# Optimization experiments

Measured on AMD Instinct MI355X. Metric: run time of the kernel, lower is better.

The kernel has to match this reference:

```python
import jax, jax.numpy as jnp
import numpy as np
from jax import lax

CONF_THRESH = 0.5   # from module __init__
NMS_THRESH = 0.4    # from module __init__
TOP_K = 1000        # static pre-NMS candidate cap (JAX needs fixed shapes)

B, N, C = 16, 22743, 80  # batch, predictions (608px, 3 scales), COCO classes


def setup_inputs() -> dict:
    key = jax.random.key(0)
    # YOLOv3 raw output: [B, N, 5+C] = (cx, cy, w, h, obj, cls_0..cls_{C-1})
    v3_out = jax.random.uniform(key, (B, N, 5 + C), dtype=jnp.float32)
    return {"v3_out": v3_out}


def _xywh2xyxy(b):
    cx, cy, w, h = b[..., 0], b[..., 1], b[..., 2], b[..., 3]
    return jnp.stack([cx - w * 0.5, cy - h * 0.5, cx + w * 0.5, cy + h * 0.5], axis=-1)


def _pairwise_iou(boxes):
    # boxes: [K, 4] in xyxy -> [K, K] IoU
    x1 = jnp.maximum(boxes[:, None, 0], boxes[None, :, 0])
    y1 = jnp.maximum(boxes[:, None, 1], boxes[None, :, 1])
    x2 = jnp.minimum(boxes[:, None, 2], boxes[None, :, 2])
    y2 = jnp.minimum(boxes[:, None, 3], boxes[None, :, 3])
    inter = jnp.clip(x2 - x1, 0.0) * jnp.clip(y2 - y1, 0.0)
    area = jnp.clip(boxes[:, 2] - boxes[:, 0], 0.0) * jnp.clip(boxes[:, 3] - boxes[:, 1], 0.0)
    union = area[:, None] + area[None, :] - inter
    return inter / (union + 1e-16)


def _nms_image(pred):
    # pred: [N, 5+C]
    boxes = _xywh2xyxy(pred[:, :4])                 # [N, 4]
    obj = pred[:, 4]
    cls_conf = jnp.max(pred[:, 5:], axis=-1)        # best class confidence
    cls_id = jnp.argmax(pred[:, 5:], axis=-1)       # best class index
    # confidence filter (obj >= thresh) folded into the sort key
    score = jnp.where(obj >= CONF_THRESH, obj * cls_conf, -1.0)
    top_score, idx = lax.top_k(score, TOP_K)        # sorted descending by score
    valid = top_score > 0.0                          # survivors of the conf filter

    boxes_k = boxes[idx]          # [K, 4]
    obj_k = obj[idx]
    conf_k = cls_conf[idx]
    cls_k = cls_id[idx]

    iou = _pairwise_iou(boxes_k)                                   # [K, K]
    suppress = (iou > NMS_THRESH) & (cls_k[:, None] == cls_k[None, :])

    # greedy NMS over the score-sorted list: box i (if kept) kills later overlaps
    later = jnp.arange(TOP_K)

    def step(i, keep):
        kill = suppress[i] & (later > i) & keep[i]
        return keep & ~kill

    keep = lax.fori_loop(0, TOP_K, step, valid)

    # detections: (x1, y1, x2, y2, obj_conf, cls_conf, cls_id), zeroed where dropped
    dets = jnp.concatenate(
        [boxes_k, obj_k[:, None], conf_k[:, None], cls_k.astype(jnp.float32)[:, None]],
        axis=-1,
    )
    return dets * keep[:, None].astype(dets.dtype)   # [K, 7]


def reference(v3_out):
    # [B, K, 7] padded detections per image (zero rows = suppressed/invalid)
    return jax.vmap(_nms_image)(v3_out)
```

## Files before the change

### kernel.cpp

```cpp
#include <hip/hip_runtime.h>
#include <cstdint>

#pragma clang fp contract(off)

constexpr int cB = 16;
constexpr int cN = 22743;
constexpr int cROW = 85;
constexpr int cK = 1000;
constexpr float CONF_T = 0.5f;
constexpr float NMS_T = 0.4f;

__global__ __launch_bounds__(256) void k_score(const float* __restrict__ in,
                                               unsigned* __restrict__ ukey) {
  __shared__ float sdata[10880];
  constexpr int F4_PER_BLK = 2720;
  constexpr int TOTAL_F4 = (cB * cN * cROW) / 4;
  int tid = threadIdx.x;
  const float4* gin4 = (const float4*)in;
  float4* s4 = (float4*)sdata;
  int base_f4 = blockIdx.x * F4_PER_BLK;
#pragma unroll
  for (int q = 0; q < 11; ++q) {
    int k = tid + 256 * q;
    if (k < F4_PER_BLK) {
      int g = base_f4 + k;
      if (g < TOTAL_F4) s4[k] = gin4[g];
    }
  }
  __syncthreads();
  int r = tid >> 1, h = tid & 1;
  int grow = blockIdx.x * 128 + r;
  if (grow < cB * cN) {
    const float* rowp = sdata + cROW * r;
    int j0 = 5 + h * 40;
    float m0 = rowp[j0 + 0], m1 = rowp[j0 + 1];
    float m2 = rowp[j0 + 2], m3 = rowp[j0 + 3];
#pragma unroll
    for (int k = 4; k < 40; k += 4) {
      m0 = fmaxf(m0, rowp[j0 + k + 0]);
      m1 = fmaxf(m1, rowp[j0 + k + 1]);
      m2 = fmaxf(m2, rowp[j0 + k + 2]);
      m3 = fmaxf(m3, rowp[j0 + k + 3]);
    }
    float m = fmaxf(fmaxf(m0, m1), fmaxf(m2, m3));
    m = fmaxf(m, __shfl_xor(m, 1));
    if (h == 0) {
      float obj = rowp[4];
      unsigned u = 0u;
      if (obj >= CONF_T) {
        float s = obj * m;
        if (s > 0.0f) u = __float_as_uint(s);
      }
      ukey[grow] = u;
    }
  }
}

__device__ __forceinline__ void sort1024_u32_asc(unsigned* a, int tid) {
  for (int k = 2; k <= 1024; k <<= 1) {
    for (int j = k >> 1; j >= 1; j >>= 1) {
      __syncthreads();
      if (tid < 512) {
        int i = ((tid & ~(j - 1)) << 1) | (tid & (j - 1));
        int p = i | j;
        unsigned x = a[i], y = a[p];
        bool up = ((i & k) == 0);
        bool sw = up ? (x > y) : (x < y);
        if (sw) { a[i] = y; a[p] = x; }
      }
    }
  }
  __syncthreads();
}

__global__ __launch_bounds__(1024) void k_topk(const unsigned* __restrict__ ukey,
                                               int* __restrict__ topidx) {
  __shared__ unsigned hist[2048];
  __shared__ unsigned wtot[16];
  __shared__ unsigned long long cand[1024];
  __shared__ unsigned eqbuf[1024];
  __shared__ unsigned sh_T, sh_newrank, sh_E, sh_cnt;
  int img = blockIdx.x;
  int tid = threadIdx.x;
  int lane = tid & 63;
  int wv = tid >> 6;
  const unsigned* uk = ukey + (size_t)img * cN;

  constexpr int NIT = (cN + 1023) / 1024;
  unsigned uv[NIT];
#pragma unroll
  for (int q = 0; q < NIT; ++q) {
    int i = q * 1024 + tid;
    uv[q] = (i < cN) ? uk[i] : 0u;
  }

  unsigned prefix = 0;
  int bits = 0;
  unsigned rank = cK;
  unsigned gtc = 0;
  unsigned E = 0;

  for (int r = 0; r < 3; ++r) {
    int nb = (r < 2) ? 11 : 10;
    int shift = 32 - bits - nb;
    hist[tid] = 0u; hist[tid + 1024] = 0u;
    __syncthreads();
#pragma unroll
    for (int q = 0; q < NIT; ++q) {
      unsigned u = uv[q];
      bool inr = (q * 1024 + tid) < cN;
      bool match = inr && (bits == 0 || (u >> (32 - bits)) == prefix);
      bool isz = match && (u == 0u);
      bool nz = match && (u != 0u);
      unsigned long long mz = __ballot(isz);
      if (isz && lane == (__ffsll((long long)mz) - 1))
        atomicAdd(&hist[0], (unsigned)__popcll(mz));
      if (nz) atomicAdd(&hist[(u >> shift) & ((1u << nb) - 1u)], 1u);
    }
    __syncthreads();
    unsigned h0 = hist[2 * tid];
    unsigned h1 = hist[2 * tid + 1];
    unsigned s2 = h0 + h1;
#pragma unroll
    for (int s = 1; s < 64; s <<= 1) {
      unsigned t = __shfl_down(s2, s);
      s2 += (lane + s < 64) ? t : 0u;
    }
    if (lane == 0) wtot[wv] = s2;
    __syncthreads();
    unsigned above = 0;
    for (int w2 = wv + 1; w2 < 16; ++w2) above += wtot[w2];
    unsigned S_even = above + s2;
    unsigned S_odd = S_even - h0;
    unsigned S_next = S_odd - h1;
    if (S_even >= rank && S_odd < rank) { sh_T = 2u * tid; sh_newrank = rank - S_odd; sh_E = h0; }
    if (S_odd >= rank && S_next < rank) { sh_T = 2u * tid + 1u; sh_newrank = rank - S_next; sh_E = h1; }
    __syncthreads();
    unsigned T = sh_T;
    unsigned nr = sh_newrank;
    E = sh_E;
    gtc += rank - nr;
    rank = nr;
    prefix = (prefix << nb) | T;
    bits += nb;
    __syncthreads();
    if (gtc + E <= 1024u) break;
  }

  bool tiepath = (gtc + E > 1024u);
  unsigned pivotLo = (bits >= 32) ? prefix : (prefix << (32 - bits));
  cand[tid] = (unsigned long long)tid;
  eqbuf[tid] = 0xFFFFFFFFu;
  if (tid == 0) sh_cnt = 0u;
  __syncthreads();

  if (!tiepath) {
#pragma unroll
    for (int q = 0; q < NIT; ++q) {
      int i = q * 1024 + tid;
      unsigned u = uv[q];
      bool m = (i < cN) && (u >= pivotLo);
      unsigned long long mb = __ballot(m);
      if (m) {
        int ldr = __ffsll((long long)mb) - 1;
        unsigned base = 0;
        if (lane == ldr) base = atomicAdd(&sh_cnt, (unsigned)__popcll(mb));
        base = __shfl(base, ldr);
        unsigned pos = base + (unsigned)__popcll(mb & ((1ull << lane) - 1ull));
        if (pos < 1024u)
          cand[pos] = ((unsigned long long)u << 32) |
                      (unsigned long long)(0xFFFFFFFFu - (unsigned)i);
      }
    }
    __syncthreads();
  } else {
    unsigned P = prefix;
#pragma unroll
    for (int q = 0; q < NIT; ++q) {
      int i = q * 1024 + tid;
      unsigned u = uv[q];
      bool gt = (i < cN) && (u > P);
      unsigned long long mb = __ballot(gt);
      if (gt) {
        int ldr = __ffsll((long long)mb) - 1;
        unsigned base = 0;
        if (lane == ldr) base = atomicAdd(&sh_cnt, (unsigned)__popcll(mb));
        base = __shfl(base, ldr);
        unsigned pos = base + (unsigned)__popcll(mb & ((1ull << lane) - 1ull));
        if (pos < 1024u)
          cand[pos] = ((unsigned long long)u << 32) |
                      (unsigned long long)(0xFFFFFFFFu - (unsigned)i);
      }
    }
    __syncthreads();
    if (tid == 0) sh_E = 0u;
    __syncthreads();
#pragma unroll
    for (int q = 0; q < NIT; ++q) {
      int i = q * 1024 + tid;
      unsigned u = uv[q];
      bool eq = (i < cN) && (u == P);
      unsigned long long mb = __ballot(eq);
      if (eq) {
        int ldr = __ffsll((long long)mb) - 1;
        unsigned base = 0;
        if (lane == ldr) base = atomicAdd(&sh_E, (unsigned)__popcll(mb));
        base = __shfl(base, ldr);
        unsigned pos = base + (unsigned)__popcll(mb & ((1ull << lane) - 1ull));
        if (pos < 1024u) eqbuf[pos] = (unsigned)i;
      }
    }
    __syncthreads();
    sort1024_u32_asc(eqbuf, tid);
    int need = (int)cK - (int)gtc;
    for (int t = tid; t < need; t += 1024) {
      unsigned idx = eqbuf[t];
      if (idx != 0xFFFFFFFFu)
        cand[gtc + (unsigned)t] = ((unsigned long long)P << 32) |
                                  (unsigned long long)(0xFFFFFFFFu - idx);
    }
    __syncthreads();
  }

  unsigned long long my = cand[tid];
  unsigned rk = 0;
#pragma unroll 8
  for (int j = 0; j < 1024; ++j) rk += (cand[j] > my) ? 1u : 0u;
  if (rk < (unsigned)cK) {
    unsigned uhi = (unsigned)(my >> 32);
    int idx = (int)(0xFFFFFFFFu - (unsigned)(my & 0xFFFFFFFFull));
    topidx[img * cK + (int)rk] = (uhi > 0u) ? idx : -1;
  }
}

__global__ __launch_bounds__(256) void k_gather(const float* __restrict__ in,
                                                const int* __restrict__ topidx,
                                                float4* __restrict__ boxes,
                                                float* __restrict__ area,
                                                float* __restrict__ objv,
                                                float* __restrict__ confv,
                                                int* __restrict__ clsv,
                                                int* __restrict__ validv) {
  int wid = (int)((blockIdx.x * 256u + threadIdx.x) >> 6);
  int lane = threadIdx.x & 63;
  if (wid >= cB * cK) return;
  int img = wid / cK;
  int idx = topidx[wid];
  if (idx < 0) {
    if (lane == 0) {
      boxes[wid] = make_float4(0.f, 0.f, 0.f, 0.f);
      area[wid] = 0.f; objv[wid] = 0.f; confv[wid] = 0.f;
      clsv[wid] = -1; validv[wid] = 0;
    }
    return;
  }
  const float* row = in + ((size_t)img * cN + (size_t)idx) * cROW;
  float v = row[5 + lane];
  int ci = lane;
  if (lane < 16) {
    float v2 = row[69 + lane];
    if (v2 > v) { v = v2; ci = 64 + lane; }
  }
#pragma unroll
  for (int m = 1; m < 64; m <<= 1) {
    float ov = __shfl_xor(v, m);
    int oc = __shfl_xor(ci, m);
    if (ov > v || (ov == v && oc < ci)) { v = ov; ci = oc; }
  }
  if (lane == 0) {
    float cx = row[0], cy = row[1], w = row[2], h = row[3], ob = row[4];
    float hw = w * 0.5f, hh = h * 0.5f;
    float x1 = cx - hw, y1 = cy - hh, x2 = cx + hw, y2 = cy + hh;
    boxes[wid] = make_float4(x1, y1, x2, y2);
    area[wid] = fmaxf(x2 - x1, 0.f) * fmaxf(y2 - y1, 0.f);
    objv[wid] = ob; confv[wid] = v; clsv[wid] = ci; validv[wid] = 1;
  }
}

__global__ __launch_bounds__(256) void k_suppress(const float4* __restrict__ boxes,
                                                  const float* __restrict__ area,
                                                  const int* __restrict__ clsv,
                                                  unsigned* __restrict__ St) {
  __shared__ float sx1[1056], sy1[1056], sx2[1056], sy2[1056], sar[1056];
  __shared__ int scls[1056];
  int img = blockIdx.x >> 7;
  int rb = (blockIdx.x & 127) * 8;
  int tid = threadIdx.x;
  for (int i = tid; i < 1024; i += 256) {
    int p = i + (i >> 5);
    if (i < cK) {
      float4 b = boxes[img * cK + i];
      sx1[p] = b.x; sy1[p] = b.y; sx2[p] = b.z; sy2[p] = b.w;
      sar[p] = area[img * cK + i];
      scls[p] = clsv[img * cK + i];
    } else {
      sx1[p] = 0.f; sy1[p] = 0.f; sx2[p] = 0.f; sy2[p] = 0.f; sar[p] = 0.f;
      scls[p] = -2;
    }
  }
  __syncthreads();
  int i = rb + (tid >> 5);
  int w = tid & 31;
  int pi = i + (i >> 5);
  float bx1 = sx1[pi], by1 = sy1[pi], bx2 = sx2[pi], by2 = sy2[pi], ba = sar[pi];
  int bc = scls[pi];
  unsigned word = 0u;
#pragma unroll 4
  for (int bit = 0; bit < 32; ++bit) {
    int pj = 33 * w + bit;
    float xx1 = fmaxf(bx1, sx1[pj]);
    float yy1 = fmaxf(by1, sy1[pj]);
    float xx2 = fminf(bx2, sx2[pj]);
    float yy2 = fminf(by2, sy2[pj]);
    float inter = fmaxf(xx2 - xx1, 0.f) * fmaxf(yy2 - yy1, 0.f);
    float uni = ba + sar[pj] - inter;
    float iou = inter / (uni + 1e-16f);
    if (iou > NMS_T && bc == scls[pj]) word |= (1u << bit);
  }
  St[((size_t)(img * 32 + w)) * 1024 + (size_t)i] = word;
}

__device__ __forceinline__ unsigned u4c(const uint4& v, int c) {
  return c == 0 ? v.x : c == 1 ? v.y : c == 2 ? v.z : v.w;
}

__device__ __forceinline__ void nms_load(const uint4* __restrict__ colv, int b,
                                         uint4 (&buf)[8]) {
#pragma unroll
  for (int q = 0; q < 8; ++q) buf[q] = colv[8 * b + q];
}

__device__ __forceinline__ void nms_proc(int b, int lane, unsigned& kw,
                                         const uint4 (&W)[8]) {
  unsigned dec = 0u;
  if (lane == b) {
    unsigned kwb = kw;
#pragma unroll
    for (int t = 0; t < 32; ++t) {
      if ((kwb >> t) & 1u) {
        dec |= (1u << t);
        unsigned rw = u4c(W[t >> 2], t & 3);
        unsigned mgt = (t == 31) ? 0u : (0xFFFFFFFFu << (t + 1));
        kwb &= ~(rw & mgt);
      }
    }
    kw = kwb;
  }
  dec = __shfl(dec, b);
  if (lane > b) {
#pragma unroll
    for (int t = 0; t < 32; ++t) {
      unsigned sel = 0u - ((dec >> t) & 1u);
      kw &= ~(u4c(W[t >> 2], t & 3) & sel);
    }
  }
}

__global__ __launch_bounds__(64) void k_nms(const unsigned* __restrict__ St,
                                            const int* __restrict__ validv,
                                            const float4* __restrict__ boxes,
                                            const float* __restrict__ objv,
                                            const float* __restrict__ confv,
                                            const int* __restrict__ clsv,
                                            float* __restrict__ out) {
  __shared__ unsigned keep_sh[32];
  int img = blockIdx.x;
  int lane = threadIdx.x;
  if (lane < 32) {
    const uint4* colv = (const uint4*)(St + ((size_t)(img * 32 + lane)) * 1024);
    unsigned kw = 0u;
    const int4* v4 = (const int4*)(validv + img * cK);
#pragma unroll
    for (int q = 0; q < 8; ++q) {
      int k0 = (lane << 5) + 4 * q;
      if (k0 < cK) {
        int4 t = v4[lane * 8 + q];
        kw |= (unsigned)(t.x != 0) << (4 * q + 0);
        kw |= (unsigned)(t.y != 0) << (4 * q + 1);
        kw |= (unsigned)(t.z != 0) << (4 * q + 2);
        kw |= (unsigned)(t.w != 0) << (4 * q + 3);
      }
    }
    uint4 bufA[8], bufB[8];
    nms_load(colv, 0, bufA);
    for (int b = 0; b < 32; b += 2) {
      if (b + 1 < 32) nms_load(colv, b + 1, bufB);
      nms_proc(b, lane, kw, bufA);
      if (b + 2 < 32) nms_load(colv, b + 2, bufA);
      nms_proc(b + 1, lane, kw, bufB);
    }
    keep_sh[lane] = kw;
  }
  __syncthreads();
  for (int k = lane; k < cK; k += 64) {
    bool kp = ((keep_sh[k >> 5] >> (k & 31)) & 1u) != 0u;
    size_t o = ((size_t)img * cK + (size_t)k) * 7;
    if (kp) {
      float4 b = boxes[img * cK + k];
      out[o + 0] = b.x; out[o + 1] = b.y; out[o + 2] = b.z; out[o + 3] = b.w;
      out[o + 4] = objv[img * cK + k];
      out[o + 5] = confv[img * cK + k];
      out[o + 6] = (float)clsv[img * cK + k];
    } else {
      out[o + 0] = 0.f; out[o + 1] = 0.f; out[o + 2] = 0.f; out[o + 3] = 0.f;
      out[o + 4] = 0.f; out[o + 5] = 0.f; out[o + 6] = 0.f;
    }
  }
}

extern "C" void kernel_launch(void* const* d_in, const int* in_sizes, int n_in,
                              void* d_out, int out_size, void* d_ws, size_t ws_size,
                              hipStream_t stream) {
  const float* in = (const float*)d_in[0];
  float* out = (float*)d_out;
  char* ws = (char*)d_ws;
  size_t off = 0;
  auto take = [&](size_t bytes) {
    size_t r = off;
    off += (bytes + 255) & ~(size_t)255;
    return r;
  };
  unsigned* ukey = (unsigned*)(ws + take((size_t)cB * cN * 4));
  int* topidx = (int*)(ws + take((size_t)cB * cK * 4));
  float4* boxes = (float4*)(ws + take((size_t)cB * cK * 16));
  float* area = (float*)(ws + take((size_t)cB * cK * 4));
  float* objv = (float*)(ws + take((size_t)cB * cK * 4));
  float* confv = (float*)(ws + take((size_t)cB * cK * 4));
  int* clsv = (int*)(ws + take((size_t)cB * cK * 4));
  int* validv = (int*)(ws + take((size_t)cB * cK * 4));
  unsigned* St = (unsigned*)(ws + take((size_t)cB * 32 * 1024 * 4));

  int nrows = cB * cN;
  int blocks1 = (nrows + 127) / 128;
  k_score<<<blocks1, 256, 0, stream>>>(in, ukey);
  k_topk<<<cB, 1024, 0, stream>>>(ukey, topidx);
  int waves3 = cB * cK;
  k_gather<<<(waves3 * 64 + 255) / 256, 256, 0, stream>>>(in, topidx, boxes, area,
                                                          objv, confv, clsv, validv);
  k_suppress<<<cB * 128, 256, 0, stream>>>(boxes, area, clsv, St);
  k_nms<<<cB, 64, 0, stream>>>(St, validv, boxes, objv, confv, clsv, out);
}
```

Baseline: 281.0 us.

## Fuse gather into top-k and NMS into suppress via last-block atomic counter

```diff
diff --git a/kernel.cpp b/kernel.cpp
--- a/kernel.cpp
+++ b/kernel.cpp
@@ -74,17 +74,28 @@
 }
 
 __global__ __launch_bounds__(1024) void k_topk(const unsigned* __restrict__ ukey,
-                                               int* __restrict__ topidx) {
+                                               const float* __restrict__ in,
+                                               int* __restrict__ topidx,
+                                               float4* __restrict__ boxes,
+                                               float* __restrict__ area,
+                                               float* __restrict__ objv,
+                                               float* __restrict__ confv,
+                                               int* __restrict__ clsv,
+                                               unsigned* __restrict__ cnt) {
   __shared__ unsigned hist[2048];
   __shared__ unsigned wtot[16];
   __shared__ unsigned long long cand[1024];
   __shared__ unsigned eqbuf[1024];
+  __shared__ unsigned praw[8][1024];
+  __shared__ int sh_topidx[1024];
   __shared__ unsigned sh_T, sh_newrank, sh_E, sh_cnt;
   int img = blockIdx.x;
   int tid = threadIdx.x;
   int lane = tid & 63;
   int wv = tid >> 6;
   const unsigned* uk = ukey + (size_t)img * cN;
+
+  if (tid == 0) cnt[img] = 0u;
 
   constexpr int NIT = (cN + 1023) / 1024;
   unsigned uv[NIT];
@@ -222,67 +233,142 @@
     __syncthreads();
   }
 
+  {
+    int kg = wv & 7, jg = wv >> 3;
+    unsigned long long myv[8];
+#pragma unroll
+    for (int m = 0; m < 8; ++m) myv[m] = cand[jg * 512 + m * 64 + lane];
+    unsigned c[8];
+#pragma unroll
+    for (int m = 0; m < 8; ++m) c[m] = 0u;
+    int k0 = kg * 128;
+#pragma unroll 4
+    for (int k = 0; k < 128; ++k) {
+      unsigned long long ck = cand[k0 + k];
+#pragma unroll
+      for (int m = 0; m < 8; ++m) c[m] += (ck > myv[m]) ? 1u : 0u;
+    }
+#pragma unroll
+    for (int m = 0; m < 8; ++m) praw[kg][jg * 512 + m * 64 + lane] = c[m];
+  }
+  __syncthreads();
+  unsigned rk = 0;
+#pragma unroll
+  for (int g = 0; g < 8; ++g) rk += praw[g][tid];
   unsigned long long my = cand[tid];
-  unsigned rk = 0;
-#pragma unroll 8
-  for (int j = 0; j < 1024; ++j) rk += (cand[j] > my) ? 1u : 0u;
+  sh_topidx[tid] = -1;
+  __syncthreads();
   if (rk < (unsigned)cK) {
     unsigned uhi = (unsigned)(my >> 32);
     int idx = (int)(0xFFFFFFFFu - (unsigned)(my & 0xFFFFFFFFull));
-    topidx[img * cK + (int)rk] = (uhi > 0u) ? idx : -1;
-  }
-}
-
-__global__ __launch_bounds__(256) void k_gather(const float* __restrict__ in,
-                                                const int* __restrict__ topidx,
-                                                float4* __restrict__ boxes,
-                                                float* __restrict__ area,
-                                                float* __restrict__ objv,
-                                                float* __restrict__ confv,
-                                                int* __restrict__ clsv,
-                                                int* __restrict__ validv) {
-  int wid = (int)((blockIdx.x * 256u + threadIdx.x) >> 6);
-  int lane = threadIdx.x & 63;
-  if (wid >= cB * cK) return;
-  int img = wid / cK;
-  int idx = topidx[wid];
-  if (idx < 0) {
+    int oi = (uhi > 0u) ? idx : -1;
+    topidx[img * cK + (int)rk] = oi;
+    sh_topidx[(int)rk] = oi;
+  }
+  __syncthreads();
+
+  for (int j = 0; j < 32; ++j) {
+    int s0 = wv + 32 * j;
+    int s1 = s0 + 16;
+    int i0 = (s0 < cK) ? sh_topidx[s0] : -1;
+    int i1 = (s1 < cK) ? sh_topidx[s1] : -1;
+    const float* r0 = in + ((size_t)img * cN + (size_t)(i0 < 0 ? 0 : i0)) * cROW;
+    const float* r1 = in + ((size_t)img * cN + (size_t)(i1 < 0 ? 0 : i1)) * cROW;
+    float va = r0[5 + lane];
+    float vb = r1[5 + lane];
+    int ca = lane, cb = lane;
+    if (lane < 16) {
+      float v2a = r0[69 + lane];
+      float v2b = r1[69 + lane];
+      if (v2a > va) { va = v2a; ca = 64 + lane; }
+      if (v2b > vb) { vb = v2b; cb = 64 + lane; }
+    }
+#pragma unroll
+    for (int m = 1; m < 64; m <<= 1) {
+      float ova = __shfl_xor(va, m); int oca = __shfl_xor(ca, m);
+      float ovb = __shfl_xor(vb, m); int ocb = __shfl_xor(cb, m);
+      if (ova > va || (ova == va && oca < ca)) { va = ova; ca = oca; }
+      if (ovb > vb || (ovb == vb && ocb < cb)) { vb = ovb; cb = ocb; }
+    }
     if (lane == 0) {
-      boxes[wid] = make_float4(0.f, 0.f, 0.f, 0.f);
-      area[wid] = 0.f; objv[wid] = 0.f; confv[wid] = 0.f;
-      clsv[wid] = -1; validv[wid] = 0;
-    }
-    return;
-  }
-  const float* row = in + ((size_t)img * cN + (size_t)idx) * cROW;
-  float v = row[5 + lane];
-  int ci = lane;
-  if (lane < 16) {
-    float v2 = row[69 + lane];
-    if (v2 > v) { v = v2; ci = 64 + lane; }
-  }
-#pragma unroll
-  for (int m = 1; m < 64; m <<= 1) {
-    float ov = __shfl_xor(v, m);
-    int oc = __shfl_xor(ci, m);
-    if (ov > v || (ov == v && oc < ci)) { v = ov; ci = oc; }
-  }
-  if (lane == 0) {
-    float cx = row[0], cy = row[1], w = row[2], h = row[3], ob = row[4];
-    float hw = w * 0.5f, hh = h * 0.5f;
-    float x1 = cx - hw, y1 = cy - hh, x2 = cx + hw, y2 = cy + hh;
-    boxes[wid] = make_float4(x1, y1, x2, y2);
-    area[wid] = fmaxf(x2 - x1, 0.f) * fmaxf(y2 - y1, 0.f);
-    objv[wid] = ob; confv[wid] = v; clsv[wid] = ci; validv[wid] = 1;
-  }
-}
-
-__global__ __launch_bounds__(256) void k_suppress(const float4* __restrict__ boxes,
-                                                  const float* __restrict__ area,
-                                                  const int* __restrict__ clsv,
-                                                  unsigned* __restrict__ St) {
+      if (s0 < cK) {
+        int wid = img * cK + s0;
+        if (i0 < 0) {
+          boxes[wid] = make_float4(0.f, 0.f, 0.f, 0.f);
+          area[wid] = 0.f; objv[wid] = 0.f; confv[wid] = 0.f; clsv[wid] = -1;
+        } else {
+          float cx = r0[0], cy = r0[1], w = r0[2], h = r0[3], ob = r0[4];
+          float hw = w * 0.5f, hh = h * 0.5f;
+          float x1 = cx - hw, y1 = cy - hh, x2 = cx + hw, y2 = cy + hh;
+          boxes[wid] = make_float4(x1, y1, x2, y2);
+          area[wid] = fmaxf(x2 - x1, 0.f) * fmaxf(y2 - y1, 0.f);
+          objv[wid] = ob; confv[wid] = va; clsv[wid] = ca;
+        }
+      }
+      if (s1 < cK) {
+        int wid = img * cK + s1;
+        if (i1 < 0) {
+          boxes[wid] = make_float4(0.f, 0.f, 0.f, 0.f);
+          area[wid] = 0.f; objv[wid] = 0.f; confv[wid] = 0.f; clsv[wid] = -1;
+        } else {
+          float cx = r1[0], cy = r1[1], w = r1[2], h = r1[3], ob = r1[4];
+          float hw = w * 0.5f, hh = h * 0.5f;
+          float x1 = cx - hw, y1 = cy - hh, x2 = cx + hw, y2 = cy + hh;
+          boxes[wid] = make_float4(x1, y1, x2, y2);
+          area[wid] = fmaxf(x2 - x1, 0.f) * fmaxf(y2 - y1, 0.f);
+          objv[wid] = ob; confv[wid] = vb; clsv[wid] = cb;
+        }
+      }
+    }
+  }
+}
+
+__device__ __forceinline__ unsigned u4c(const uint4& v, int c) {
+  return c == 0 ? v.x : c == 1 ? v.y : c == 2 ? v.z : v.w;
+}
+
+__device__ __forceinline__ void nms_load(const uint4* __restrict__ colv, int b,
+                                         uint4 (&buf)[8]) {
+#pragma unroll
+  for (int q = 0; q < 8; ++q) buf[q] = colv[8 * b + q];
+}
+
+__device__ __forceinline__ void nms_proc(int b, int lane, unsigned& kw,
+                                         const uint4 (&W)[8]) {
+  unsigned dec = 0u;
+  if (lane == b) {
+    unsigned kwb = kw;
+#pragma unroll
+    for (int t = 0; t < 32; ++t) {
+      if ((kwb >> t) & 1u) {
+        dec |= (1u << t);
+        unsigned rw = u4c(W[t >> 2], t & 3);
+        unsigned mgt = (t == 31) ? 0u : (0xFFFFFFFFu << (t + 1));
+        kwb &= ~(rw & mgt);
+      }
+    }
+    kw = kwb;
+  }
+  dec = __shfl(dec, b);
+  if (dec != 0u && lane > b) {
+#pragma unroll
+    for (int t = 0; t < 32; ++t) {
+      unsigned sel = 0u - ((dec >> t) & 1u);
+      kw &= ~(u4c(W[t >> 2], t & 3) & sel);
+    }
+  }
+}
+
+__global__ __launch_bounds__(256) void k_suppress_nms(
+    const float4* __restrict__ boxes, const float* __restrict__ area,
+    const int* __restrict__ clsv, const float* __restrict__ objv,
+    const float* __restrict__ confv, const int* __restrict__ topidx,
+    unsigned* __restrict__ St, unsigned* __restrict__ cnt,
+    float* __restrict__ out) {
   __shared__ float sx1[1056], sy1[1056], sx2[1056], sy2[1056], sar[1056];
   __shared__ int scls[1056];
+  __shared__ unsigned sh_old;
+  __shared__ unsigned keep_sh[32];
   int img = blockIdx.x >> 7;
   int rb = (blockIdx.x & 127) * 8;
   int tid = threadIdx.x;
@@ -299,100 +385,64 @@
     }
   }
   __syncthreads();
-  int i = rb + (tid >> 5);
-  int w = tid & 31;
-  int pi = i + (i >> 5);
-  float bx1 = sx1[pi], by1 = sy1[pi], bx2 = sx2[pi], by2 = sy2[pi], ba = sar[pi];
-  int bc = scls[pi];
-  unsigned word = 0u;
+  {
+    int i = rb + (tid >> 5);
+    int w = tid & 31;
+    int pi = i + (i >> 5);
+    float bx1 = sx1[pi], by1 = sy1[pi], bx2 = sx2[pi], by2 = sy2[pi], ba = sar[pi];
+    int bc = scls[pi];
+    unsigned word = 0u;
 #pragma unroll 4
-  for (int bit = 0; bit < 32; ++bit) {
-    int pj = 33 * w + bit;
-    float xx1 = fmaxf(bx1, sx1[pj]);
-    float yy1 = fmaxf(by1, sy1[pj]);
-    float xx2 = fminf(bx2, sx2[pj]);
-    float yy2 = fminf(by2, sy2[pj]);
-    float inter = fmaxf(xx2 - xx1, 0.f) * fmaxf(yy2 - yy1, 0.f);
-    float uni = ba + sar[pj] - inter;
-    float iou = inter / (uni + 1e-16f);
-    if (iou > NMS_T && bc == scls[pj]) word |= (1u << bit);
-  }
-  St[((size_t)(img * 32 + w)) * 1024 + (size_t)i] = word;
-}
-
-__device__ __forceinline__ unsigned u4c(const uint4& v, int c) {
-  return c == 0 ? v.x : c == 1 ? v.y : c == 2 ? v.z : v.w;
-}
-
-__device__ __forceinline__ void nms_load(const uint4* __restrict__ colv, int b,
-                                         uint4 (&buf)[8]) {
-#pragma unroll
-  for (int q = 0; q < 8; ++q) buf[q] = colv[8 * b + q];
-}
-
-__device__ __forceinline__ void nms_proc(int b, int lane, unsigned& kw,
-                                         const uint4 (&W)[8]) {
-  unsigned dec = 0u;
-  if (lane == b) {
-    unsigned kwb = kw;
-#pragma unroll
-    for (int t = 0; t < 32; ++t) {
-      if ((kwb >> t) & 1u) {
-        dec |= (1u << t);
-        unsigned rw = u4c(W[t >> 2], t & 3);
-        unsigned mgt = (t == 31) ? 0u : (0xFFFFFFFFu << (t + 1));
-        kwb &= ~(rw & mgt);
-      }
-    }
-    kw = kwb;
-  }
-  dec = __shfl(dec, b);
-  if (lane > b) {
-#pragma unroll
-    for (int t = 0; t < 32; ++t) {
-      unsigned sel = 0u - ((dec >> t) & 1u);
-      kw &= ~(u4c(W[t >> 2], t & 3) & sel);
-    }
-  }
-}
-
-__global__ __launch_bounds__(64) void k_nms(const unsigned* __restrict__ St,
-                                            const int* __restrict__ validv,
-                                            const float4* __restrict__ boxes,
-                                            const float* __restrict__ objv,
-                                            const float* __restrict__ confv,
-                                            const int* __restrict__ clsv,
-                                            float* __restrict__ out) {
-  __shared__ unsigned keep_sh[32];
-  int img = blockIdx.x;
-  int lane = threadIdx.x;
-  if (lane < 32) {
-    const uint4* colv = (const uint4*)(St + ((size_t)(img * 32 + lane)) * 1024);
+    for (int bit = 0; bit < 32; ++bit) {
+      int pj = 33 * w + bit;
+      float xx1 = fmaxf(bx1, sx1[pj]);
+      float yy1 = fmaxf(by1, sy1[pj]);
+      float xx2 = fminf(bx2, sx2[pj]);
+      float yy2 = fminf(by2, sy2[pj]);
+      float inter = fmaxf(xx2 - xx1, 0.f) * fmaxf(yy2 - yy1, 0.f);
+      float uni = ba + sar[pj] - inter;
+      float iou = inter / (uni + 1e-16f);
+      if (iou > NMS_T && bc == scls[pj]) word |= (1u << bit);
+    }
+    St[((size_t)(img * 32 + w)) * 1024 + (size_t)i] = word;
+  }
+  __syncthreads();
+  if (tid == 0) {
+    __threadfence();
+    sh_old = atomicAdd(&cnt[img], 1u);
+  }
+  __syncthreads();
+  if (sh_old != 127u) return;
+  if (tid == 0) __threadfence();
+  __syncthreads();
+
+  if (tid < 32) {
+    const uint4* colv = (const uint4*)(St + ((size_t)(img * 32 + tid)) * 1024);
     unsigned kw = 0u;
-    const int4* v4 = (const int4*)(validv + img * cK);
+    const int4* v4 = (const int4*)(topidx + img * cK);
 #pragma unroll
     for (int q = 0; q < 8; ++q) {
-      int k0 = (lane << 5) + 4 * q;
+      int k0 = (tid << 5) + 4 * q;
       if (k0 < cK) {
-        int4 t = v4[lane * 8 + q];
-        kw |= (unsigned)(t.x != 0) << (4 * q + 0);
-        kw |= (unsigned)(t.y != 0) << (4 * q + 1);
-        kw |= (unsigned)(t.z != 0) << (4 * q + 2);
-        kw |= (unsigned)(t.w != 0) << (4 * q + 3);
+        int4 t = v4[tid * 8 + q];
+        kw |= (unsigned)(t.x >= 0) << (4 * q + 0);
+        kw |= (unsigned)(t.y >= 0) << (4 * q + 1);
+        kw |= (unsigned)(t.z >= 0) << (4 * q + 2);
+        kw |= (unsigned)(t.w >= 0) << (4 * q + 3);
       }
     }
     uint4 bufA[8], bufB[8];
     nms_load(colv, 0, bufA);
     for (int b = 0; b < 32; b += 2) {
       if (b + 1 < 32) nms_load(colv, b + 1, bufB);
-      nms_proc(b, lane, kw, bufA);
+      nms_proc(b, tid, kw, bufA);
       if (b + 2 < 32) nms_load(colv, b + 2, bufA);
-      nms_proc(b + 1, lane, kw, bufB);
-    }
-    keep_sh[lane] = kw;
-  }
-  __syncthreads();
-  for (int k = lane; k < cK; k += 64) {
+      nms_proc(b + 1, tid, kw, bufB);
+    }
+    keep_sh[tid] = kw;
+  }
+  __syncthreads();
+  for (int k = tid; k < cK; k += 256) {
     bool kp = ((keep_sh[k >> 5] >> (k & 31)) & 1u) != 0u;
     size_t o = ((size_t)img * cK + (size_t)k) * 7;
     if (kp) {
@@ -427,16 +477,14 @@
   float* objv = (float*)(ws + take((size_t)cB * cK * 4));
   float* confv = (float*)(ws + take((size_t)cB * cK * 4));
   int* clsv = (int*)(ws + take((size_t)cB * cK * 4));
-  int* validv = (int*)(ws + take((size_t)cB * cK * 4));
   unsigned* St = (unsigned*)(ws + take((size_t)cB * 32 * 1024 * 4));
+  unsigned* cnt = (unsigned*)(ws + take((size_t)cB * 4));
 
   int nrows = cB * cN;
   int blocks1 = (nrows + 127) / 128;
   k_score<<<blocks1, 256, 0, stream>>>(in, ukey);
-  k_topk<<<cB, 1024, 0, stream>>>(ukey, topidx);
-  int waves3 = cB * cK;
-  k_gather<<<(waves3 * 64 + 255) / 256, 256, 0, stream>>>(in, topidx, boxes, area,
-                                                          objv, confv, clsv, validv);
-  k_suppress<<<cB * 128, 256, 0, stream>>>(boxes, area, clsv, St);
-  k_nms<<<cB, 64, 0, stream>>>(St, validv, boxes, objv, confv, clsv, out);
-}
+  k_topk<<<cB, 1024, 0, stream>>>(ukey, in, topidx, boxes, area, objv, confv,
+                                  clsv, cnt);
+  k_suppress_nms<<<cB * 128, 256, 0, stream>>>(boxes, area, clsv, objv, confv,
+                                               topidx, St, cnt, out);
+}
```

After: 405.2 us. +44.2%, slower.
